# Kernel tuning notes

Measured on AMD Instinct MI355X. Metric: run time of the kernel, lower is better.

## Reference

```python
import jax, jax.numpy as jnp
import numpy as np

H = 96
NH = 4
HD = H // NH
SPARSITY = 0.5
LN_EPS = 1e-5


def _lstm_layer(xs, w_ih, w_hh, b_ih, b_hh):
    # xs: [B, T, I]; PyTorch gate order i, f, g, o
    B = xs.shape[0]
    Hd = w_hh.shape[1]
    def step(carry, x_t):
        h, c = carry
        gates = x_t @ w_ih.T + h @ w_hh.T + b_ih + b_hh  # [B, 4H]
        i, f, g, o = jnp.split(gates, 4, axis=-1)
        i = jax.nn.sigmoid(i); f = jax.nn.sigmoid(f)
        g = jnp.tanh(g); o = jax.nn.sigmoid(o)
        c = f * c + i * g
        h = o * jnp.tanh(c)
        return (h, c), h
    h0 = jnp.zeros((B, Hd), xs.dtype)
    c0 = jnp.zeros((B, Hd), xs.dtype)
    _, hs = jax.lax.scan(step, (h0, c0), xs.transpose(1, 0, 2))  # [T, B, H]
    return hs.transpose(1, 0, 2)


def _layer_norm(x, w, b):
    mu = jnp.mean(x, axis=-1, keepdims=True)
    var = jnp.mean((x - mu) ** 2, axis=-1, keepdims=True)
    return (x - mu) * jax.lax.rsqrt(var + LN_EPS) * w + b


def _split_heads(x, B, T):
    return x.reshape(B, T, NH, HD).transpose(0, 2, 1, 3)  # [B, H, T, d]


def _sparse_attention(x, qw, kw, vw, ow):
    B, T, _ = x.shape
    q = _split_heads(x @ qw.T, B, T)
    k = _split_heads(x @ kw.T, B, T)
    v = _split_heads(x @ vw.T, B, T)
    scores = jnp.einsum('bhtd,bhsd->bhts', q, k) / np.sqrt(HD).astype(np.float32)
    num_keep = int(T * SPARSITY)
    topv, _ = jax.lax.top_k(scores, num_keep)
    kth = topv[..., -1:]  # threshold == k-th largest (equiv to topk+scatter mask for distinct values)
    scores = jnp.where(scores >= kth, scores, -jnp.inf)
    attn = jax.nn.softmax(scores, axis=-1)  # dropout is identity in eval
    out = jnp.einsum('bhts,bhsd->bhtd', attn, v)
    out = out.transpose(0, 2, 1, 3).reshape(B, T, H)
    return out @ ow.T


def _mha(x, in_w, in_b, out_w, out_b):
    B, T, _ = x.shape
    qkv = x @ in_w.T + in_b  # [B, T, 3H]
    q, k, v = jnp.split(qkv, 3, axis=-1)
    q = _split_heads(q, B, T); k = _split_heads(k, B, T); v = _split_heads(v, B, T)
    scores = jnp.einsum('bhtd,bhsd->bhts', q, k) / np.sqrt(HD).astype(np.float32)
    attn = jax.nn.softmax(scores, axis=-1)
    out = jnp.einsum('bhts,bhsd->bhtd', attn, v)
    out = out.transpose(0, 2, 1, 3).reshape(B, T, H)
    return out @ out_w.T + out_b


def _encoder_layer(x, in_w, in_b, out_w, out_b, l1_w, l1_b, l2_w, l2_b, ln1_w, ln1_b, ln2_w, ln2_b):
    # PyTorch TransformerEncoderLayer, post-norm, ReLU, eval (no dropout)
    x = _layer_norm(x + _mha(x, in_w, in_b, out_w, out_b), ln1_w, ln1_b)
    ff = jax.nn.relu(x @ l1_w.T + l1_b) @ l2_w.T + l2_b
    return _layer_norm(x + ff, ln2_w, ln2_b)


def setup_inputs() -> dict:
    key = jax.random.key(0)
    ks = iter(jax.random.split(key, 40))
    B, T, I = 16, 1024, 64
    FF = 2 * H
    def rnd(shape, scale=0.05):
        return (jax.random.normal(next(ks), shape, dtype=jnp.float32) * scale)
    inp = {
        'x': jax.random.normal(next(ks), (B, T, I), dtype=jnp.float32),
        'w_ih0': rnd((4 * H, I)), 'w_hh0': rnd((4 * H, H)),
        'b_ih0': rnd((4 * H,)), 'b_hh0': rnd((4 * H,)),
        'w_ih1': rnd((4 * H, H)), 'w_hh1': rnd((4 * H, H)),
        'b_ih1': rnd((4 * H,)), 'b_hh1': rnd((4 * H,)),
        'qw': rnd((H, H)), 'kw': rnd((H, H)), 'vw': rnd((H, H)), 'ow': rnd((H, H)),
        'enc_in_w': rnd((2, 3 * H, H)), 'enc_in_b': rnd((2, 3 * H)),
        'enc_out_w': rnd((2, H, H)), 'enc_out_b': rnd((2, H)),
        'enc_l1_w': rnd((2, FF, H)), 'enc_l1_b': rnd((2, FF)),
        'enc_l2_w': rnd((2, H, FF)), 'enc_l2_b': rnd((2, H)),
        'enc_ln1_w': jnp.ones((2, H), jnp.float32), 'enc_ln1_b': jnp.zeros((2, H), jnp.float32),
        'enc_ln2_w': jnp.ones((2, H), jnp.float32), 'enc_ln2_b': jnp.zeros((2, H), jnp.float32),
        'fc_w': rnd((1, H)), 'fc_b': rnd((1,)),
    }
    return inp


def reference(x, w_ih0, w_hh0, b_ih0, b_hh0, w_ih1, w_hh1, b_ih1, b_hh1,
              qw, kw, vw, ow,
              enc_in_w, enc_in_b, enc_out_w, enc_out_b,
              enc_l1_w, enc_l1_b, enc_l2_w, enc_l2_b,
              enc_ln1_w, enc_ln1_b, enc_ln2_w, enc_ln2_b,
              fc_w, fc_b):
    h = _lstm_layer(x, w_ih0, w_hh0, b_ih0, b_hh0)
    h = _lstm_layer(h, w_ih1, w_hh1, b_ih1, b_hh1)
    h = _sparse_attention(h, qw, kw, vw, ow)
    for i in range(2):
        h = _encoder_layer(h, enc_in_w[i], enc_in_b[i], enc_out_w[i], enc_out_b[i],
                           enc_l1_w[i], enc_l1_b[i], enc_l2_w[i], enc_l2_b[i],
                           enc_ln1_w[i], enc_ln1_b[i], enc_ln2_w[i], enc_ln2_b[i])
    return h[:, -1, :] @ fc_w.T + fc_b  # [B, 1]
```

## Files before the change

kernel.cpp:

```cpp
#include <hip/hip_runtime.h>
#include <cstdint>
#include <cmath>

#define T_SEQ 1024
#define BATCH 16
#define HID 96
#define G4 384
#define QKV_LD 288
#define HDIM 24
#define KKEEP 512
#define SCALE 0.20412414523193154f
#define L2E 1.4426950408889634f

typedef _Float16 half2v __attribute__((ext_vector_type(2)));
typedef __bf16 bf16x8 __attribute__((ext_vector_type(8)));
typedef float  f32x4v __attribute__((ext_vector_type(4)));

__device__ __forceinline__ float wred_sum(float v){
#pragma unroll
  for (int o=32;o;o>>=1) v += __shfl_xor(v,o,64);
  return v;
}
__device__ __forceinline__ float wred_max(float v){
#pragma unroll
  for (int o=32;o;o>>=1) v = fmaxf(v,__shfl_xor(v,o,64));
  return v;
}
__device__ __forceinline__ int wred_sumi(int v){
#pragma unroll
  for (int o=32;o;o>>=1) v += __shfl_xor(v,o,64);
  return v;
}
__device__ __forceinline__ unsigned fmono(float f){
  unsigned u = __float_as_uint(f);
  return (u & 0x80000000u) ? ~u : (u | 0x80000000u);
}
__device__ __forceinline__ float sigf(float x){
  return __builtin_amdgcn_rcpf(1.f + __builtin_amdgcn_exp2f(-L2E*x));
}
__device__ __forceinline__ float tanhf2(float x){
  return fmaf(-2.f, __builtin_amdgcn_rcpf(1.f + __builtin_amdgcn_exp2f((2.f*L2E)*x)), 1.f);
}
template<int CTRL>
__device__ __forceinline__ float dpp_add_f(float v){
  int s = __builtin_amdgcn_update_dpp(0, __float_as_int(v), CTRL, 0xF, 0xF, true);
  return v + __int_as_float(s);
}
__device__ __forceinline__ float dpp_red4(float v){
  v = dpp_add_f<0xB1>(v);
  v = dpp_add_f<0x4E>(v);
  return v;
}
#if __has_builtin(__builtin_amdgcn_fdot2)
__device__ __forceinline__ float fdot2(half2v a, half2v b, float c){
  return __builtin_amdgcn_fdot2(a, b, c, false);
}
#else
__device__ __forceinline__ float fdot2(half2v a, half2v b, float c){
  return fmaf((float)a[0], (float)b[0], fmaf((float)a[1], (float)b[1], c));
}
#endif
__device__ __forceinline__ unsigned short f2bf(float f){
  unsigned u = __float_as_uint(f);
  return (unsigned short)((u + 0x7fffu + ((u>>16)&1u)) >> 16);
}
__device__ __forceinline__ f32x4v mfma16(uint4 a, uint4 b, f32x4v c){
  return __builtin_amdgcn_mfma_f32_16x16x32_bf16(
      __builtin_bit_cast(bf16x8, a), __builtin_bit_cast(bf16x8, b), c, 0, 0, 0);
}

template<int K>
__global__ __launch_bounds__(256)
void gemm_mfma(const float* __restrict__ A, const float* __restrict__ W,
               const float* __restrict__ b1, const float* __restrict__ b2,
               float* __restrict__ C, int N, int ldc, int coff, int relu)
{
  __shared__ unsigned short As[128][K+8];
  __shared__ unsigned short Ws[64][K+8];
  const int tid = threadIdx.x;
  const int wave = tid >> 6, lane = tid & 63;
  const int ln = lane & 15, kq = lane >> 4;
  const int m0 = blockIdx.y * 128, n0 = blockIdx.x * 64;

  for (int idx = tid; idx < 128*(K/4); idx += 256){
    const int row = idx / (K/4), c4 = idx - row*(K/4);
    const float4 v = *(const float4*)(A + (size_t)(m0+row)*K + c4*4);
    ushort4 s = {f2bf(v.x), f2bf(v.y), f2bf(v.z), f2bf(v.w)};
    *(ushort4*)&As[row][c4*4] = s;
  }
  for (int idx = tid; idx < 64*(K/4); idx += 256){
    const int row = idx / (K/4), c4 = idx - row*(K/4);
    float4 v = {0,0,0,0};
    const int gn = n0 + row;
    if (gn < N) v = *(const float4*)(W + (size_t)gn*K + c4*4);
    ushort4 s = {f2bf(v.x), f2bf(v.y), f2bf(v.z), f2bf(v.w)};
    *(ushort4*)&Ws[row][c4*4] = s;
  }
  __syncthreads();

  f32x4v acc[2][4];
#pragma unroll
  for (int mi=0;mi<2;++mi)
#pragma unroll
    for (int ni=0;ni<4;++ni){ f32x4v z = {0.f,0.f,0.f,0.f}; acc[mi][ni] = z; }

#pragma unroll
  for (int ks=0; ks<K/32; ++ks){
    uint4 af[2], bf[4];
#pragma unroll
    for (int mi=0;mi<2;++mi)
      af[mi] = *(const uint4*)&As[wave*32 + mi*16 + ln][ks*32 + kq*8];
#pragma unroll
    for (int ni=0;ni<4;++ni)
      bf[ni] = *(const uint4*)&Ws[ni*16 + ln][ks*32 + kq*8];
#pragma unroll
    for (int mi=0;mi<2;++mi)
#pragma unroll
      for (int ni=0;ni<4;++ni)
        acc[mi][ni] = mfma16(af[mi], bf[ni], acc[mi][ni]);
  }

#pragma unroll
  for (int ni=0;ni<4;++ni){
    const int gn = n0 + ni*16 + ln;
    if (gn >= N) continue;
    float bias = 0.f;
    if (b1) bias += b1[gn];
    if (b2) bias += b2[gn];
#pragma unroll
    for (int mi=0;mi<2;++mi){
      const int row = m0 + wave*32 + mi*16 + kq*4;
#pragma unroll
      for (int r=0;r<4;++r){
        float v = acc[mi][ni][r] + bias;
        if (relu) v = fmaxf(v, 0.f);
        C[(size_t)(row + r)*ldc + coff + gn] = v;
      }
    }
  }
}

__global__ __launch_bounds__(256)
void pack_qkv_kernel(const float* __restrict__ qw, const float* __restrict__ kw,
                     const float* __restrict__ vw, float* __restrict__ wqkv)
{
  const int i = blockIdx.x*256 + threadIdx.x;
  if (i < 9216)       wqkv[i] = qw[i];
  else if (i < 18432) wqkv[i] = kw[i-9216];
  else if (i < 27648) wqkv[i] = vw[i-18432];
}

__global__ __launch_bounds__(384)
void lstm_kernel(const float* __restrict__ pre, const float* __restrict__ w_hh,
                 float* __restrict__ hout)
{
  const int b = blockIdx.x;
  const int tid = threadIdx.x;
  const int q = tid & 3, j = tid >> 2;
  half2v w[4][12];
#pragma unroll
  for (int g=0; g<4; ++g){
    const float* wp = w_hh + (size_t)(g*96 + j)*96 + q*24;
#pragma unroll
    for (int k=0;k<12;++k){
      half2v t; t[0] = (_Float16)wp[2*k]; t[1] = (_Float16)wp[2*k+1];
      w[g][k] = t;
    }
  }
  __shared__ _Float16 h_lds[96];
  float c = 0.f;
  if (tid < 96) h_lds[tid] = (_Float16)0.f;
  __syncthreads();

  const float* prow = pre + (size_t)b*T_SEQ*G4 + q*96 + j;
  float* hrow = hout + (size_t)b*T_SEQ*HID;
  float pf[4];
#pragma unroll
  for (int i=0;i<4;++i) pf[i] = prow[(size_t)i*G4];

  for (int tb=0; tb<T_SEQ; tb+=4){
#pragma unroll
    for (int u=0; u<4; ++u){
      const int t = tb + u;
      const float pcur = pf[u];
      int tn = t + 4; if (tn > T_SEQ-1) tn = T_SEQ-1;
      pf[u] = prow[(size_t)tn*G4];
      const uint4 a0 = *(const uint4*)(h_lds + q*24);
      const uint4 a1 = *(const uint4*)(h_lds + q*24 + 8);
      const uint4 a2 = *(const uint4*)(h_lds + q*24 + 16);
      half2v h2[12];
      h2[0]=__builtin_bit_cast(half2v, a0.x); h2[1]=__builtin_bit_cast(half2v, a0.y);
      h2[2]=__builtin_bit_cast(half2v, a0.z); h2[3]=__builtin_bit_cast(half2v, a0.w);
      h2[4]=__builtin_bit_cast(half2v, a1.x); h2[5]=__builtin_bit_cast(half2v, a1.y);
      h2[6]=__builtin_bit_cast(half2v, a1.z); h2[7]=__builtin_bit_cast(half2v, a1.w);
      h2[8]=__builtin_bit_cast(half2v, a2.x); h2[9]=__builtin_bit_cast(half2v, a2.y);
      h2[10]=__builtin_bit_cast(half2v, a2.z); h2[11]=__builtin_bit_cast(half2v, a2.w);

      float sA0=0.f,sA1=0.f,sA2=0.f,sA3=0.f;
      float sB0=0.f,sB1=0.f,sB2=0.f,sB3=0.f;
#pragma unroll
      for (int k=0;k<12;k+=2){
        sA0 = fdot2(w[0][k], h2[k], sA0);  sB0 = fdot2(w[0][k+1], h2[k+1], sB0);
        sA1 = fdot2(w[1][k], h2[k], sA1);  sB1 = fdot2(w[1][k+1], h2[k+1], sB1);
        sA2 = fdot2(w[2][k], h2[k], sA2);  sB2 = fdot2(w[2][k+1], h2[k+1], sB2);
        sA3 = fdot2(w[3][k], h2[k], sA3);  sB3 = fdot2(w[3][k+1], h2[k+1], sB3);
      }
      float s0 = sA0+sB0, s1 = sA1+sB1, s2 = sA2+sB2, s3 = sA3+sB3;
      s0 += (q==0) ? pcur : 0.f;
      s1 += (q==1) ? pcur : 0.f;
      s2 += (q==2) ? pcur : 0.f;
      s3 += (q==3) ? pcur : 0.f;
      s0 = dpp_red4(s0);
      s1 = dpp_red4(s1);
      s2 = dpp_red4(s2);
      s3 = dpp_red4(s3);
      const float iv = sigf(s0), fv = sigf(s1);
      const float gv = tanhf2(s2), ov = sigf(s3);
      c = fmaf(fv, c, iv*gv);
      const float hv = ov * tanhf2(c);
      if (q == 0){
        h_lds[j] = (_Float16)hv;
        hrow[t*HID + j] = hv;
      }
      __syncthreads();
    }
  }
}

__global__ __launch_bounds__(512)
void attn_kernel(const float* __restrict__ qkv, float* __restrict__ out, int sparse)
{
  __shared__ float kl[24][260];
  const int tid = threadIdx.x;
  const int wave = tid >> 6, lane = tid & 63;
  const int bh = blockIdx.x >> 7;
  const int b = bh >> 2, h = bh & 3;
  const int tq = ((blockIdx.x & 127) << 3) + wave;
  const size_t base = (size_t)b * T_SEQ;
  const int hoff = h * HDIM;
  float q[24];
  {
    const float* qp = qkv + (base + tq)*QKV_LD + hoff;
#pragma unroll
    for (int d4=0; d4<6; ++d4){
      float4 t = *(const float4*)(qp + d4*4);
      q[d4*4]=t.x; q[d4*4+1]=t.y; q[d4*4+2]=t.z; q[d4*4+3]=t.w;
    }
  }
  float sc[16];
  for (int c=0;c<4;++c){
    __syncthreads();
#pragma unroll
    for (int rep=0;rep<3;++rep){
      int p = rep*512 + tid;
      int sl = p/6, d4 = p - sl*6;
      const float4 kv = *(const float4*)(qkv + (base + (c<<8) + sl)*QKV_LD + 96 + hoff + d4*4);
      kl[d4*4+0][sl]=kv.x; kl[d4*4+1][sl]=kv.y; kl[d4*4+2][sl]=kv.z; kl[d4*4+3][sl]=kv.w;
    }
    __syncthreads();
    float a0=0.f,a1=0.f,a2=0.f,a3=0.f;
#pragma unroll
    for (int d=0; d<24; ++d){
      const float4 kd = *(const float4*)&kl[d][lane*4];
      a0 += q[d]*kd.x; a1 += q[d]*kd.y; a2 += q[d]*kd.z; a3 += q[d]*kd.w;
    }
    sc[c*4+0]=a0*SCALE; sc[c*4+1]=a1*SCALE; sc[c*4+2]=a2*SCALE; sc[c*4+3]=a3*SCALE;
  }
  float m_loc = sc[0];
#pragma unroll
  for (int i=1;i<16;++i) m_loc = fmaxf(m_loc, sc[i]);
  const float m = wred_max(m_loc);
  float sum_loc = 0.f;
  if (sparse){
    unsigned u[16];
#pragma unroll
    for (int i=0;i<16;++i) u[i] = fmono(sc[i]);
    unsigned prefix = 0;
    for (int bit=31; bit>=0; --bit){
      unsigned test = prefix | (1u<<bit);
      int cnt = 0;
#pragma unroll
      for (int i=0;i<16;++i) cnt += (u[i] >= test) ? 1 : 0;
      cnt = wred_sumi(cnt);
      if (cnt >= KKEEP) prefix = test;
    }
#pragma unroll
    for (int i=0;i<16;++i){
      float e = (u[i] >= prefix) ? __expf(sc[i]-m) : 0.f;
      sc[i] = e; sum_loc += e;
    }
  } else {
#pragma unroll
    for (int i=0;i<16;++i){
      float e = __expf(sc[i]-m);
      sc[i] = e; sum_loc += e;
    }
  }
  const float inv = 1.f / wred_sum(sum_loc);
#pragma unroll
  for (int i=0;i<16;++i) sc[i] *= inv;
  float acc[24] = {};
  for (int c=0;c<4;++c){
    __syncthreads();
#pragma unroll
    for (int rep=0;rep<3;++rep){
      int p = rep*512 + tid;
      int sl = p/6, d4 = p - sl*6;
      const float4 vv = *(const float4*)(qkv + (base + (c<<8) + sl)*QKV_LD + 192 + hoff + d4*4);
      kl[d4*4+0][sl]=vv.x; kl[d4*4+1][sl]=vv.y; kl[d4*4+2][sl]=vv.z; kl[d4*4+3][sl]=vv.w;
    }
    __syncthreads();
    const float w0=sc[c*4], w1=sc[c*4+1], w2=sc[c*4+2], w3=sc[c*4+3];
#pragma unroll
    for (int d=0; d<24; ++d){
      const float4 vd = *(const float4*)&kl[d][lane*4];
      acc[d] += w0*vd.x + w1*vd.y + w2*vd.z + w3*vd.w;
    }
  }
#pragma unroll
  for (int d=0; d<24; ++d) acc[d] = wred_sum(acc[d]);
  if (lane == 0){
    float* op = out + (base + tq)*HID + hoff;
#pragma unroll
    for (int d4=0; d4<6; ++d4){
      float4 t = {acc[d4*4], acc[d4*4+1], acc[d4*4+2], acc[d4*4+3]};
      *(float4*)(op + d4*4) = t;
    }
  }
}

__global__ __launch_bounds__(64)
void attn_last_kernel(const float* __restrict__ qkv, float* __restrict__ out)
{
  const int bh = blockIdx.x, b = bh>>2, h = bh&3;
  const int lane = threadIdx.x;
  const size_t base = (size_t)b*T_SEQ;
  const int hoff = h*HDIM;
  float q[24];
  {
    const float* qp = qkv + (base + T_SEQ-1)*QKV_LD + hoff;
#pragma unroll
    for (int d4=0; d4<6; ++d4){
      float4 t = *(const float4*)(qp + d4*4);
      q[d4*4]=t.x; q[d4*4+1]=t.y; q[d4*4+2]=t.z; q[d4*4+3]=t.w;
    }
  }
  float sc[16];
#pragma unroll 4
  for (int i=0;i<16;++i){
    const float* kp = qkv + (base + i*64 + lane)*QKV_LD + 96 + hoff;
    float a = 0.f;
#pragma unroll
    for (int d4=0; d4<6; ++d4){
      float4 kv = *(const float4*)(kp + d4*4);
      a += q[d4*4]*kv.x + q[d4*4+1]*kv.y + q[d4*4+2]*kv.z + q[d4*4+3]*kv.w;
    }
    sc[i] = a*SCALE;
  }
  float m_loc = sc[0];
#pragma unroll
  for (int i=1;i<16;++i) m_loc = fmaxf(m_loc, sc[i]);
  const float m = wred_max(m_loc);
  float sum_loc = 0.f;
#pragma unroll
  for (int i=0;i<16;++i){ sc[i] = __expf(sc[i]-m); sum_loc += sc[i]; }
  const float inv = 1.f / wred_sum(sum_loc);
  float acc[24] = {};
#pragma unroll 4
  for (int i=0;i<16;++i){
    const float* vp = qkv + (base + i*64 + lane)*QKV_LD + 192 + hoff;
    const float wgt = sc[i]*inv;
#pragma unroll
    for (int d4=0; d4<6; ++d4){
      float4 vv = *(const float4*)(vp + d4*4);
      acc[d4*4]   += wgt*vv.x; acc[d4*4+1] += wgt*vv.y;
      acc[d4*4+2] += wgt*vv.z; acc[d4*4+3] += wgt*vv.w;
    }
  }
#pragma unroll
  for (int d=0; d<24; ++d) acc[d] = wred_sum(acc[d]);
  if (lane == 0){
    float* op = out + (base + T_SEQ-1)*HID + hoff;
#pragma unroll
    for (int d4=0; d4<6; ++d4){
      float4 t = {acc[d4*4], acc[d4*4+1], acc[d4*4+2], acc[d4*4+3]};
      *(float4*)(op + d4*4) = t;
    }
  }
}

__global__ __launch_bounds__(256)
void resln_kernel(const float* __restrict__ x, const float* __restrict__ y,
                  const float* __restrict__ w, const float* __restrict__ bb,
                  float* __restrict__ out)
{
  const int row = blockIdx.x*4 + (threadIdx.x>>6);
  const int lane = threadIdx.x & 63;
  const float* xr = x + (size_t)row*HID;
  const float* yr = y + (size_t)row*HID;
  float v0 = xr[lane] + yr[lane];
  float v1 = (lane < 32) ? (xr[64+lane] + yr[64+lane]) : 0.f;
  float mu = wred_sum(v0+v1) * (1.f/96.f);
  float d0 = v0-mu, d1 = (lane<32) ? (v1-mu) : 0.f;
  float var = wred_sum(d0*d0 + d1*d1) * (1.f/96.f);
  float rs = rsqrtf(var + 1e-5f);
  float* orow = out + (size_t)row*HID;
  orow[lane] = d0*rs*w[lane] + bb[lane];
  if (lane < 32) orow[64+lane] = d1*rs*w[64+lane] + bb[64+lane];
}

__device__ __forceinline__ float block_sum_192(float v, float* red){
  v = wred_sum(v);
  const int tid = threadIdx.x;
  if ((tid & 63) == 0) red[tid>>6] = v;
  __syncthreads();
  float r = red[0]+red[1]+red[2];
  __syncthreads();
  return r;
}

__global__ __launch_bounds__(192)
void tail_kernel(const float* __restrict__ xin, const float* __restrict__ mha,
                 const float* __restrict__ out_w, const float* __restrict__ out_b,
                 const float* __restrict__ l1_w, const float* __restrict__ l1_b,
                 const float* __restrict__ l2_w, const float* __restrict__ l2_b,
                 const float* __restrict__ ln1w, const float* __restrict__ ln1b,
                 const float* __restrict__ ln2w, const float* __restrict__ ln2b,
                 const float* __restrict__ fcw, const float* __restrict__ fcb,
                 float* __restrict__ outp)
{
  const int b = blockIdx.x, tid = threadIdx.x;
  __shared__ float y[96], f1[192], mrow[96], red[3];
  const size_t row = ((size_t)b*T_SEQ + T_SEQ-1)*HID;
  if (tid < 96) mrow[tid] = mha[row + tid];
  __syncthreads();
  float r = 0.f;
  if (tid < 96){
    float p = out_b[tid];
    const float* wr = out_w + tid*96;
#pragma unroll 4
    for (int d=0; d<96; ++d) p += mrow[d]*wr[d];
    r = xin[row + tid] + p;
  }
  float mu = block_sum_192(tid<96 ? r : 0.f, red) * (1.f/96.f);
  float dv = tid<96 ? r-mu : 0.f;
  float var = block_sum_192(dv*dv, red) * (1.f/96.f);
  float rs = rsqrtf(var + 1e-5f);
  if (tid < 96) y[tid] = dv*rs*ln1w[tid] + ln1b[tid];
  __syncthreads();
  {
    float a = l1_b[tid];
    const float* wr = l1_w + tid*96;
#pragma unroll 4
    for (int d=0; d<96; ++d) a += y[d]*wr[d];
    f1[tid] = fmaxf(a, 0.f);
  }
  __syncthreads();
  float r2 = 0.f;
  if (tid < 96){
    float a = l2_b[tid];
    const float* wr = l2_w + tid*192;
#pragma unroll 4
    for (int d=0; d<192; ++d) a += f1[d]*wr[d];
    r2 = y[tid] + a;
  }
  float mu2 = block_sum_192(tid<96 ? r2 : 0.f, red) * (1.f/96.f);
  float dv2 = tid<96 ? r2-mu2 : 0.f;
  float var2 = block_sum_192(dv2*dv2, red) * (1.f/96.f);
  float rs2 = rsqrtf(var2 + 1e-5f);
  float z = tid<96 ? (dv2*rs2*ln2w[tid] + ln2b[tid]) : 0.f;
  float tot = block_sum_192(tid<96 ? z*fcw[tid] : 0.f, red);
  if (tid == 0) outp[b] = tot + fcb[0];
}

extern "C" void kernel_launch(void* const* d_in, const int* in_sizes, int n_in,
                              void* d_out, int out_size, void* d_ws, size_t ws_size,
                              hipStream_t stream)
{
  const float* x     = (const float*)d_in[0];
  const float* w_ih0 = (const float*)d_in[1];
  const float* w_hh0 = (const float*)d_in[2];
  const float* b_ih0 = (const float*)d_in[3];
  const float* b_hh0 = (const float*)d_in[4];
  const float* w_ih1 = (const float*)d_in[5];
  const float* w_hh1 = (const float*)d_in[6];
  const float* b_ih1 = (const float*)d_in[7];
  const float* b_hh1 = (const float*)d_in[8];
  const float* qw = (const float*)d_in[9];
  const float* kw = (const float*)d_in[10];
  const float* vw = (const float*)d_in[11];
  const float* ow = (const float*)d_in[12];
  const float* enc_in_w  = (const float*)d_in[13];
  const float* enc_in_b  = (const float*)d_in[14];
  const float* enc_out_w = (const float*)d_in[15];
  const float* enc_out_b = (const float*)d_in[16];
  const float* enc_l1_w  = (const float*)d_in[17];
  const float* enc_l1_b  = (const float*)d_in[18];
  const float* enc_l2_w  = (const float*)d_in[19];
  const float* enc_l2_b  = (const float*)d_in[20];
  const float* enc_ln1_w = (const float*)d_in[21];
  const float* enc_ln1_b = (const float*)d_in[22];
  const float* enc_ln2_w = (const float*)d_in[23];
  const float* enc_ln2_b = (const float*)d_in[24];
  const float* fc_w = (const float*)d_in[25];
  const float* fc_b = (const float*)d_in[26];
  float* outp = (float*)d_out;

  float* ws = (float*)d_ws;
  const size_t MT = (size_t)BATCH*T_SEQ;
  float* pre  = ws;
  float* bufA = pre  + MT*G4;
  float* bufB = bufA + MT*HID;
  float* bufC = bufB + MT*HID;
  float* wqkv = bufC + MT*HID;

  auto gemm = [&](const float* A, const float* W, const float* bb1, const float* bb2,
                  float* C, int N, int K, int ldc, int coff, int relu){
    dim3 grid((N+63)/64, 128);
    if (K == 64)
      gemm_mfma<64><<<grid, dim3(256), 0, stream>>>(A, W, bb1, bb2, C, N, ldc, coff, relu);
    else if (K == 96)
      gemm_mfma<96><<<grid, dim3(256), 0, stream>>>(A, W, bb1, bb2, C, N, ldc, coff, relu);
    else
      gemm_mfma<192><<<grid, dim3(256), 0, stream>>>(A, W, bb1, bb2, C, N, ldc, coff, relu);
  };

  pack_qkv_kernel<<<dim3(108), dim3(256), 0, stream>>>(qw, kw, vw, wqkv);

  gemm(x, w_ih0, b_ih0, b_hh0, pre, 384, 64, 384, 0, 0);
  lstm_kernel<<<dim3(BATCH), dim3(384), 0, stream>>>(pre, w_hh0, bufA);
  gemm(bufA, w_ih1, b_ih1, b_hh1, pre, 384, 96, 384, 0, 0);
  lstm_kernel<<<dim3(BATCH), dim3(384), 0, stream>>>(pre, w_hh1, bufB);
  gemm(bufB, wqkv, nullptr, nullptr, pre, 288, 96, QKV_LD, 0, 0);
  attn_kernel<<<dim3(8192), dim3(512), 0, stream>>>(pre, bufA, 1);
  gemm(bufA, ow, nullptr, nullptr, bufB, 96, 96, 96, 0, 0);
  gemm(bufB, enc_in_w, enc_in_b, nullptr, pre, 288, 96, QKV_LD, 0, 0);
  attn_kernel<<<dim3(8192), dim3(512), 0, stream>>>(pre, bufA, 0);
  gemm(bufA, enc_out_w, enc_out_b, nullptr, bufC, 96, 96, 96, 0, 0);
  resln_kernel<<<dim3(4096), dim3(256), 0, stream>>>(bufB, bufC, enc_ln1_w, enc_ln1_b, bufB);
  gemm(bufB, enc_l1_w, enc_l1_b, nullptr, pre, 192, 96, 192, 0, 1);
  gemm(pre, enc_l2_w, enc_l2_b, nullptr, bufC, 96, 192, 96, 0, 0);
  resln_kernel<<<dim3(4096), dim3(256), 0, stream>>>(bufB, bufC, enc_ln2_w, enc_ln2_b, bufB);
  gemm(bufB, enc_in_w + 288*96, enc_in_b + 288, nullptr, pre, 288, 96, QKV_LD, 0, 0);
  attn_last_kernel<<<dim3(64), dim3(64), 0, stream>>>(pre, bufA);
  tail_kernel<<<dim3(BATCH), dim3(192), 0, stream>>>(
      bufB, bufA,
      enc_out_w + 96*96, enc_out_b + 96,
      enc_l1_w + 192*96, enc_l1_b + 192,
      enc_l2_w + 96*192, enc_l2_b + 96,
      enc_ln1_w + 96, enc_ln1_b + 96,
      enc_ln2_w + 96, enc_ln2_b + 96,
      fc_w, fc_b, outp);
}
```

Measured before the change: 1.999 ms.

## Fuse both LSTM layers into one wavefront-pipelined kernel

Merges the two sequential LSTM layer kernels and the intermediate input-projection GEMM into one 768-thread kernel. Layer 0 runs on half the threads while layer 1 runs one timestep behind on the other half, computing its input projection in fp32 from layer-0 h held in double-buffered LDS. This aims to roughly halve the serial recurrence time by overlapping the two scans and to drop a GEMM launch plus its global round trip. In exchange, layer-1 threads do more work per step (an extra 96-wide fp32 dot per gate with weights kept in registers), so register pressure rises and the per-step critical path may lengthen.

```diff
diff --git a/kernel.cpp b/kernel.cpp
--- a/kernel.cpp
+++ b/kernel.cpp
@@ -68,6 +68,17 @@
   return __builtin_amdgcn_mfma_f32_16x16x32_bf16(
       __builtin_bit_cast(bf16x8, a), __builtin_bit_cast(bf16x8, b), c, 0, 0, 0);
 }
+__device__ __forceinline__ void load12h2(const _Float16* p, half2v* h2){
+  const uint4 a0 = *(const uint4*)(p);
+  const uint4 a1 = *(const uint4*)(p + 8);
+  const uint4 a2 = *(const uint4*)(p + 16);
+  h2[0]=__builtin_bit_cast(half2v, a0.x); h2[1]=__builtin_bit_cast(half2v, a0.y);
+  h2[2]=__builtin_bit_cast(half2v, a0.z); h2[3]=__builtin_bit_cast(half2v, a0.w);
+  h2[4]=__builtin_bit_cast(half2v, a1.x); h2[5]=__builtin_bit_cast(half2v, a1.y);
+  h2[6]=__builtin_bit_cast(half2v, a1.z); h2[7]=__builtin_bit_cast(half2v, a1.w);
+  h2[8]=__builtin_bit_cast(half2v, a2.x); h2[9]=__builtin_bit_cast(half2v, a2.y);
+  h2[10]=__builtin_bit_cast(half2v, a2.z); h2[11]=__builtin_bit_cast(half2v, a2.w);
+}
 
 template<int K>
 __global__ __launch_bounds__(256)
@@ -150,79 +161,145 @@
   else if (i < 27648) wqkv[i] = vw[i-18432];
 }
 
-__global__ __launch_bounds__(384)
-void lstm_kernel(const float* __restrict__ pre, const float* __restrict__ w_hh,
-                 float* __restrict__ hout)
-{
-  const int b = blockIdx.x;
-  const int tid = threadIdx.x;
-  const int q = tid & 3, j = tid >> 2;
-  half2v w[4][12];
-#pragma unroll
-  for (int g=0; g<4; ++g){
-    const float* wp = w_hh + (size_t)(g*96 + j)*96 + q*24;
-#pragma unroll
-    for (int k=0;k<12;++k){
-      half2v t; t[0] = (_Float16)wp[2*k]; t[1] = (_Float16)wp[2*k+1];
-      w[g][k] = t;
-    }
-  }
-  __shared__ _Float16 h_lds[96];
+__global__ __launch_bounds__(768)
+void lstm_fused_kernel(const float* __restrict__ pre0,
+                       const float* __restrict__ w_hh0,
+                       const float* __restrict__ w_ih1,
+                       const float* __restrict__ w_hh1,
+                       const float* __restrict__ b_ih1,
+                       const float* __restrict__ b_hh1,
+                       float* __restrict__ hout)
+{
+  const int b = blockIdx.x, tid = threadIdx.x;
+  const bool isL1 = tid >= 384;
+  const int lt = isL1 ? (tid - 384) : tid;
+  const int q = lt & 3, j = lt >> 2;
+
+  half2v wh[4][12];
+  {
+    const float* src = isL1 ? w_hh1 : w_hh0;
+#pragma unroll
+    for (int g=0; g<4; ++g){
+      const float* wp = src + (size_t)(g*96 + j)*96 + q*24;
+#pragma unroll
+      for (int k=0;k<12;++k){
+        half2v t; t[0] = (_Float16)wp[2*k]; t[1] = (_Float16)wp[2*k+1];
+        wh[g][k] = t;
+      }
+    }
+  }
+  float wf[4][24];
+  float bias1[4] = {0,0,0,0};
+  if (isL1){
+#pragma unroll
+    for (int g=0; g<4; ++g){
+      const float* wp = w_ih1 + (size_t)(g*96 + j)*96 + q*24;
+#pragma unroll
+      for (int k=0;k<24;++k) wf[g][k] = wp[k];
+      bias1[g] = b_ih1[g*96 + j] + b_hh1[g*96 + j];
+    }
+  }
+
+  __shared__ _Float16 h0h[2][96];
+  __shared__ float    h0f[2][96];
+  __shared__ _Float16 h1h[2][96];
+  if (tid < 96){
+    h0h[0][tid] = (_Float16)0.f; h0h[1][tid] = (_Float16)0.f;
+    h0f[0][tid] = 0.f;           h0f[1][tid] = 0.f;
+    h1h[0][tid] = (_Float16)0.f; h1h[1][tid] = (_Float16)0.f;
+  }
   float c = 0.f;
-  if (tid < 96) h_lds[tid] = (_Float16)0.f;
-  __syncthreads();
-
-  const float* prow = pre + (size_t)b*T_SEQ*G4 + q*96 + j;
+  const float* prow = pre0 + (size_t)b*T_SEQ*G4 + q*96 + j;
   float* hrow = hout + (size_t)b*T_SEQ*HID;
   float pf[4];
-#pragma unroll
-  for (int i=0;i<4;++i) pf[i] = prow[(size_t)i*G4];
-
-  for (int tb=0; tb<T_SEQ; tb+=4){
+  if (!isL1){
+#pragma unroll
+    for (int i=0;i<4;++i) pf[i] = prow[(size_t)i*G4];
+  }
+  __syncthreads();
+
+  for (int tb=0; tb<1028; tb+=4){
 #pragma unroll
     for (int u=0; u<4; ++u){
-      const int t = tb + u;
-      const float pcur = pf[u];
-      int tn = t + 4; if (tn > T_SEQ-1) tn = T_SEQ-1;
-      pf[u] = prow[(size_t)tn*G4];
-      const uint4 a0 = *(const uint4*)(h_lds + q*24);
-      const uint4 a1 = *(const uint4*)(h_lds + q*24 + 8);
-      const uint4 a2 = *(const uint4*)(h_lds + q*24 + 16);
-      half2v h2[12];
-      h2[0]=__builtin_bit_cast(half2v, a0.x); h2[1]=__builtin_bit_cast(half2v, a0.y);
-      h2[2]=__builtin_bit_cast(half2v, a0.z); h2[3]=__builtin_bit_cast(half2v, a0.w);
-      h2[4]=__builtin_bit_cast(half2v, a1.x); h2[5]=__builtin_bit_cast(half2v, a1.y);
-      h2[6]=__builtin_bit_cast(half2v, a1.z); h2[7]=__builtin_bit_cast(half2v, a1.w);
-      h2[8]=__builtin_bit_cast(half2v, a2.x); h2[9]=__builtin_bit_cast(half2v, a2.y);
-      h2[10]=__builtin_bit_cast(half2v, a2.z); h2[11]=__builtin_bit_cast(half2v, a2.w);
-
-      float sA0=0.f,sA1=0.f,sA2=0.f,sA3=0.f;
-      float sB0=0.f,sB1=0.f,sB2=0.f,sB3=0.f;
-#pragma unroll
-      for (int k=0;k<12;k+=2){
-        sA0 = fdot2(w[0][k], h2[k], sA0);  sB0 = fdot2(w[0][k+1], h2[k+1], sB0);
-        sA1 = fdot2(w[1][k], h2[k], sA1);  sB1 = fdot2(w[1][k+1], h2[k+1], sB1);
-        sA2 = fdot2(w[2][k], h2[k], sA2);  sB2 = fdot2(w[2][k+1], h2[k+1], sB2);
-        sA3 = fdot2(w[3][k], h2[k], sA3);  sB3 = fdot2(w[3][k+1], h2[k+1], sB3);
+      const int I = tb + u;
+      if (I <= 1024){
+        if (!isL1){
+          if (I <= 1023){
+            const float pcur = pf[u];
+            int tn = I + 4; if (tn > T_SEQ-1) tn = T_SEQ-1;
+            pf[u] = prow[(size_t)tn*G4];
+            half2v h2[12];
+            load12h2(&h0h[(I+1)&1][q*24], h2);
+            float sA0=0.f,sA1=0.f,sA2=0.f,sA3=0.f;
+            float sB0=0.f,sB1=0.f,sB2=0.f,sB3=0.f;
+#pragma unroll
+            for (int k=0;k<12;k+=2){
+              sA0 = fdot2(wh[0][k], h2[k], sA0);  sB0 = fdot2(wh[0][k+1], h2[k+1], sB0);
+              sA1 = fdot2(wh[1][k], h2[k], sA1);  sB1 = fdot2(wh[1][k+1], h2[k+1], sB1);
+              sA2 = fdot2(wh[2][k], h2[k], sA2);  sB2 = fdot2(wh[2][k+1], h2[k+1], sB2);
+              sA3 = fdot2(wh[3][k], h2[k], sA3);  sB3 = fdot2(wh[3][k+1], h2[k+1], sB3);
+            }
+            float s0 = sA0+sB0, s1 = sA1+sB1, s2 = sA2+sB2, s3 = sA3+sB3;
+            s0 += (q==0) ? pcur : 0.f;
+            s1 += (q==1) ? pcur : 0.f;
+            s2 += (q==2) ? pcur : 0.f;
+            s3 += (q==3) ? pcur : 0.f;
+            s0 = dpp_red4(s0); s1 = dpp_red4(s1);
+            s2 = dpp_red4(s2); s3 = dpp_red4(s3);
+            const float iv = sigf(s0), fv = sigf(s1);
+            const float gv = tanhf2(s2), ov = sigf(s3);
+            c = fmaf(fv, c, iv*gv);
+            const float hv = ov * tanhf2(c);
+            if (q == 0){
+              h0h[I&1][j] = (_Float16)hv;
+              h0f[I&1][j] = hv;
+            }
+          }
+        } else {
+          if (I >= 1){
+            const int rb = (I+1)&1;
+            float h0v[24];
+#pragma unroll
+            for (int k4=0;k4<6;++k4){
+              const float4 t = *(const float4*)&h0f[rb][q*24 + k4*4];
+              h0v[k4*4]=t.x; h0v[k4*4+1]=t.y; h0v[k4*4+2]=t.z; h0v[k4*4+3]=t.w;
+            }
+            half2v h2b[12];
+            load12h2(&h1h[I&1][q*24], h2b);
+            float sI0=0.f,sI1=0.f,sI2=0.f,sI3=0.f;
+#pragma unroll
+            for (int k=0;k<24;++k){
+              const float h = h0v[k];
+              sI0 = fmaf(wf[0][k], h, sI0);
+              sI1 = fmaf(wf[1][k], h, sI1);
+              sI2 = fmaf(wf[2][k], h, sI2);
+              sI3 = fmaf(wf[3][k], h, sI3);
+            }
+            float rA0=0.f,rA1=0.f,rA2=0.f,rA3=0.f;
+            float rB0=0.f,rB1=0.f,rB2=0.f,rB3=0.f;
+#pragma unroll
+            for (int k=0;k<12;k+=2){
+              rA0 = fdot2(wh[0][k], h2b[k], rA0);  rB0 = fdot2(wh[0][k+1], h2b[k+1], rB0);
+              rA1 = fdot2(wh[1][k], h2b[k], rA1);  rB1 = fdot2(wh[1][k+1], h2b[k+1], rB1);
+              rA2 = fdot2(wh[2][k], h2b[k], rA2);  rB2 = fdot2(wh[2][k+1], h2b[k+1], rB2);
+              rA3 = fdot2(wh[3][k], h2b[k], rA3);  rB3 = fdot2(wh[3][k+1], h2b[k+1], rB3);
+            }
+            const float s0 = dpp_red4(sI0 + rA0 + rB0) + bias1[0];
+            const float s1 = dpp_red4(sI1 + rA1 + rB1) + bias1[1];
+            const float s2 = dpp_red4(sI2 + rA2 + rB2) + bias1[2];
+            const float s3 = dpp_red4(sI3 + rA3 + rB3) + bias1[3];
+            const float iv = sigf(s0), fv = sigf(s1);
+            const float gv = tanhf2(s2), ov = sigf(s3);
+            c = fmaf(fv, c, iv*gv);
+            const float hv = ov * tanhf2(c);
+            if (q == 0){
+              h1h[(I+1)&1][j] = (_Float16)hv;
+              hrow[(size_t)(I-1)*HID + j] = hv;
+            }
+          }
+        }
+        __syncthreads();
       }
-      float s0 = sA0+sB0, s1 = sA1+sB1, s2 = sA2+sB2, s3 = sA3+sB3;
-      s0 += (q==0) ? pcur : 0.f;
-      s1 += (q==1) ? pcur : 0.f;
-      s2 += (q==2) ? pcur : 0.f;
-      s3 += (q==3) ? pcur : 0.f;
-      s0 = dpp_red4(s0);
-      s1 = dpp_red4(s1);
-      s2 = dpp_red4(s2);
-      s3 = dpp_red4(s3);
-      const float iv = sigf(s0), fv = sigf(s1);
-      const float gv = tanhf2(s2), ov = sigf(s3);
-      c = fmaf(fv, c, iv*gv);
-      const float hv = ov * tanhf2(c);
-      if (q == 0){
-        h_lds[j] = (_Float16)hv;
-        hrow[t*HID + j] = hv;
-      }
-      __syncthreads();
     }
   }
 }
@@ -528,9 +605,8 @@
   pack_qkv_kernel<<<dim3(108), dim3(256), 0, stream>>>(qw, kw, vw, wqkv);
 
   gemm(x, w_ih0, b_ih0, b_hh0, pre, 384, 64, 384, 0, 0);
-  lstm_kernel<<<dim3(BATCH), dim3(384), 0, stream>>>(pre, w_hh0, bufA);
-  gemm(bufA, w_ih1, b_ih1, b_hh1, pre, 384, 96, 384, 0, 0);
-  lstm_kernel<<<dim3(BATCH), dim3(384), 0, stream>>>(pre, w_hh1, bufB);
+  lstm_fused_kernel<<<dim3(BATCH), dim3(768), 0, stream>>>(
+      pre, w_hh0, w_ih1, w_hh1, b_ih1, b_hh1, bufB);
   gemm(bufB, wqkv, nullptr, nullptr, pre, 288, 96, QKV_LD, 0, 0);
   attn_kernel<<<dim3(8192), dim3(512), 0, stream>>>(pre, bufA, 1);
   gemm(bufA, ow, nullptr, nullptr, bufB, 96, 96, 96, 0, 0);
```

After: 2.706 ms. 35.4% more time.
